# Optimization experiments

Hardware: AMD Instinct MI355X
Metric: run time of the kernel (lower is better)

## Reference

```python
import jax, jax.numpy as jnp
import numpy as np

N_RAYS = 131072
N_SAMPLES = 128
FEAT_DIM = 3
FAR_DELTA = 1e10  # sentinel delta appended for the last sample, as in the torch code


def setup_inputs() -> dict:
    key = jax.random.key(0)
    k1, k2, k3 = jax.random.split(key, 3)
    # densities are non-negative (output of e.g. relu/softplus in NeRF)
    density = jax.random.uniform(k1, (N_RAYS, N_SAMPLES), dtype=jnp.float32) * 2.0
    feature = jax.random.uniform(k2, (N_RAYS, N_SAMPLES, FEAT_DIM), dtype=jnp.float32)
    # monotonically increasing per-ray sample depths: near + cumsum(uniform bins)
    bins = jax.random.uniform(k3, (N_RAYS, N_SAMPLES), dtype=jnp.float32) * 0.05 + 0.01
    depth_values = 1.0 + jnp.cumsum(bins, axis=1)
    return {"density": density, "feature": feature, "depth_values": depth_values}


def reference(density, feature, depth_values):
    # deltas: consecutive depth differences, with a huge last delta (torch.cat(..., 1e10*ones))
    deltas = jnp.concatenate(
        [depth_values[:, 1:] - depth_values[:, :-1],
         jnp.full_like(depth_values[:, :1], FAR_DELTA)],
        axis=-1,
    )  # [N, S]
    att = jnp.exp(-density * deltas)              # exp(-sigma_i * delta_i), [N, S]
    # inclusive prefix product, matching the loop: T[i] = T[i-1]*exp(-sigma_i*delta_i)
    T = jnp.cumprod(att, axis=1)                  # [N, S]
    weights = T * (1.0 - att)                     # [N, S]
    feat_out = jnp.einsum("ns,nsc->nc", weights, feature)      # [N, 3]
    depth_out = jnp.sum(weights * depth_values, axis=1)         # [N]
    return feat_out, depth_out
```

## Files before the change

### kernel.cpp

```cpp
#include <hip/hip_runtime.h>

#define N_RAYS    131072
#define N_SAMPLES 128
#define FAR_DELTA 1e10f

__global__ __launch_bounds__(256) void VolumeRenderer_57612691308835_kernel(
    const float* __restrict__ density,
    const float* __restrict__ feature,
    const float* __restrict__ depth,
    float* __restrict__ out_feat,
    float* __restrict__ out_depth)
{
    const int wave = threadIdx.x >> 6;
    const int lane = threadIdx.x & 63;
    const int ray  = (blockIdx.x << 2) + wave;
    if (ray >= N_RAYS) return;

    const int  s0   = lane << 1;
    const long base = (long)ray * N_SAMPLES;

    const float2 den = *(const float2*)(density + base + s0);
    const float2 dep = *(const float2*)(depth   + base + s0);
    const float* fp  = feature + (base + s0) * 3;
    const float2 f01 = *(const float2*)(fp);
    const float2 f23 = *(const float2*)(fp + 2);
    const float2 f45 = *(const float2*)(fp + 4);

    const float d_next = __shfl_down(dep.x, 1);
    const float delta0 = dep.y - dep.x;
    const float delta1 = (lane == 63) ? FAR_DELTA : (d_next - dep.y);

    const float att0 = __expf(-den.x * delta0);
    const float att1 = __expf(-den.y * delta1);

    float scan = att0 * att1;
    #pragma unroll
    for (int off = 1; off < 64; off <<= 1) {
        const float v = __shfl_up(scan, off);
        scan *= (lane >= off) ? v : 1.0f;
    }
    float excl = __shfl_up(scan, 1);
    if (lane == 0) excl = 1.0f;

    const float T0 = excl * att0;
    const float T1 = T0   * att1;
    const float w0 = T0 * (1.0f - att0);
    const float w1 = T1 * (1.0f - att1);

    float fx = w0 * f01.x + w1 * f23.y;
    float fy = w0 * f01.y + w1 * f45.x;
    float fz = w0 * f23.x + w1 * f45.y;
    float dd = w0 * dep.x + w1 * dep.y;

    #pragma unroll
    for (int off = 32; off >= 1; off >>= 1) {
        fx += __shfl_xor(fx, off);
        fy += __shfl_xor(fy, off);
        fz += __shfl_xor(fz, off);
        dd += __shfl_xor(dd, off);
    }

    if (lane == 0) {
        out_feat[ray * 3 + 0] = fx;
        out_feat[ray * 3 + 1] = fy;
        out_feat[ray * 3 + 2] = fz;
        out_depth[ray]        = dd;
    }
}

extern "C" void kernel_launch(void* const* d_in, const int* in_sizes, int n_in,
                              void* d_out, int out_size, void* d_ws, size_t ws_size,
                              hipStream_t stream) {
    const float* density = (const float*)d_in[0];
    const float* feature = (const float*)d_in[1];
    const float* depth   = (const float*)d_in[2];

    float* out_feat  = (float*)d_out;
    float* out_depth = (float*)d_out + (long)N_RAYS * 3;

    const int rays_per_block = 4;
    const int grid = N_RAYS / rays_per_block;
    VolumeRenderer_57612691308835_kernel<<<grid, 256, 0, stream>>>(
        density, feature, depth, out_feat, out_depth);
}
```

Before: 349.9 us.

## Rewrite renderer as persistent waves with LDS transpose, DPP scans and double-buffered loads

Each wave now handles 32 rays over 8 iterations, issuing coalesced float4 global loads that are double-buffered in registers and transposed through LDS so each lane owns 8 contiguous samples. The per-ray scan and reduction run across 16-lane rows using DPP row shifts instead of 64-lane shuffles, and the four outputs are spread across lanes so they are stored in parallel. This aims to cut load instruction count, shuffle latency and per-block launch overhead. In exchange it uses a lot of LDS per block and adds bank-padding complexity.

```diff
diff --git a/kernel.cpp b/kernel.cpp
--- a/kernel.cpp
+++ b/kernel.cpp
@@ -4,68 +4,174 @@
 #define N_SAMPLES 128
 #define FAR_DELTA 1e10f
 
-__global__ __launch_bounds__(256) void VolumeRenderer_57612691308835_kernel(
+#define NBLOCKS   1024
+
+#define ROW_SHL(n) (0x100 + (n))
+#define ROW_SHR(n) (0x110 + (n))
+#define QPERM(a,b,c,d) ((a) | ((b) << 2) | ((c) << 4) | ((d) << 6))
+
+template <int CTRL>
+__device__ __forceinline__ float dpp_f(float v, float ident) {
+    return __int_as_float(__builtin_amdgcn_update_dpp(
+        __float_as_int(ident), __float_as_int(v), CTRL, 0xF, 0xF, false));
+}
+
+#define WAVE_LDS  13312
+#define FEAT_STR  112
+#define DD_STR    48
+#define DEN_OFF   7168
+#define DEP_OFF   10240
+
+__device__ __forceinline__ int feat_woff(int lane, int c) {
+    const int q  = c * 64 + lane;
+    const int gg = q / 96;
+    const int r  = q - gg * 96;
+    const int pp = r / 6;
+    const int cc = r - pp * 6;
+    return gg * (16 * FEAT_STR) + pp * FEAT_STR + cc * 16;
+}
+__device__ __forceinline__ int dd_woff(int lane, int c, int regionOff) {
+    const int q  = c * 64 + lane;
+    const int gg = q >> 5;
+    const int r  = q & 31;
+    const int pp = r >> 1;
+    const int cc = r & 1;
+    return regionOff + gg * (16 * DD_STR) + pp * DD_STR + cc * 16;
+}
+
+
+#define LOADM(F0,F1,F2,F3,F4,F5,DN0,DN1,DP0,DP1,IT) do {                     \
+    const int fo_ = (IT) * 384, dd_ = (IT) * 128;                            \
+    F0 = fG[fo_];       F1 = fG[fo_ + 64];   F2 = fG[fo_ + 128];             \
+    F3 = fG[fo_ + 192]; F4 = fG[fo_ + 256];  F5 = fG[fo_ + 320];             \
+    DN0 = dnG[dd_];     DN1 = dnG[dd_ + 64];                                 \
+    DP0 = dpG[dd_];     DP1 = dpG[dd_ + 64];                                 \
+} while (0)
+
+#define PROCM(F0,F1,F2,F3,F4,F5,DN0,DN1,DP0,DP1,IT) do {                     \
+    \
+    *(float4*)(wlds + wf0) = F0;  *(float4*)(wlds + wf1) = F1;               \
+    *(float4*)(wlds + wf2) = F2;  *(float4*)(wlds + wf3) = F3;               \
+    *(float4*)(wlds + wf4) = F4;  *(float4*)(wlds + wf5) = F5;               \
+    *(float4*)(wlds + wdn0) = DN0; *(float4*)(wlds + wdn1) = DN1;            \
+    *(float4*)(wlds + wdp0) = DP0; *(float4*)(wlds + wdp1) = DP1;            \
+                  \
+    const float4 dn0 = *(const float4*)(dnR);                                \
+    const float4 dn1 = *(const float4*)(dnR + 16);                           \
+    const float4 dp0 = *(const float4*)(dpR);                                \
+    const float4 dp1 = *(const float4*)(dpR + 16);                           \
+    const float4 f0 = *(const float4*)(fR);                                  \
+    const float4 f1 = *(const float4*)(fR + 16);                             \
+    const float4 f2 = *(const float4*)(fR + 32);                             \
+    const float4 f3 = *(const float4*)(fR + 48);                             \
+    const float4 f4 = *(const float4*)(fR + 64);                             \
+    const float4 f5 = *(const float4*)(fR + 80);                             \
+        \
+    const float dnext = dpp_f<ROW_SHL(1)>(dp0.x, 0.0f);                      \
+    const float d7 = (p == 15) ? FAR_DELTA : (dnext - dp1.w);                \
+    const float a0 = __expf(-dn0.x * (dp0.y - dp0.x));                       \
+    const float a1 = __expf(-dn0.y * (dp0.z - dp0.y));                       \
+    const float a2 = __expf(-dn0.z * (dp0.w - dp0.z));                       \
+    const float a3 = __expf(-dn0.w * (dp1.x - dp0.w));                       \
+    const float a4 = __expf(-dn1.x * (dp1.y - dp1.x));                       \
+    const float a5 = __expf(-dn1.y * (dp1.z - dp1.y));                       \
+    const float a6 = __expf(-dn1.z * (dp1.w - dp1.z));                       \
+    const float a7 = __expf(-dn1.w * d7);                                    \
+    \
+    float s = ((a0 * a1) * (a2 * a3)) * ((a4 * a5) * (a6 * a7));             \
+    s *= dpp_f<ROW_SHR(1)>(s, 1.0f);                                         \
+    s *= dpp_f<ROW_SHR(2)>(s, 1.0f);                                         \
+    s *= dpp_f<ROW_SHR(4)>(s, 1.0f);                                         \
+    s *= dpp_f<ROW_SHR(8)>(s, 1.0f);                                         \
+    float T = dpp_f<ROW_SHR(1)>(s, 1.0f);        \
+    T *= a0; const float w0 = T * (1.0f - a0);                               \
+    T *= a1; const float w1 = T * (1.0f - a1);                               \
+    T *= a2; const float w2 = T * (1.0f - a2);                               \
+    T *= a3; const float w3 = T * (1.0f - a3);                               \
+    T *= a4; const float w4 = T * (1.0f - a4);                               \
+    T *= a5; const float w5 = T * (1.0f - a5);                               \
+    T *= a6; const float w6 = T * (1.0f - a6);                               \
+    T *= a7; const float w7 = T * (1.0f - a7);                               \
+    float fx = w0*f0.x + w1*f0.w + w2*f1.z + w3*f2.y                         \
+             + w4*f3.x + w5*f3.w + w6*f4.z + w7*f5.y;                        \
+    float fy = w0*f0.y + w1*f1.x + w2*f1.w + w3*f2.z                         \
+             + w4*f3.y + w5*f4.x + w6*f4.w + w7*f5.z;                        \
+    float fz = w0*f0.z + w1*f1.y + w2*f2.x + w3*f2.w                         \
+             + w4*f3.z + w5*f4.y + w6*f5.x + w7*f5.w;                        \
+    float dd = w0*dp0.x + w1*dp0.y + w2*dp0.z + w3*dp0.w                     \
+             + w4*dp1.x + w5*dp1.y + w6*dp1.z + w7*dp1.w;                    \
+                \
+    fx += dpp_f<ROW_SHL(8)>(fx, 0.0f);                                       \
+    fy += dpp_f<ROW_SHL(8)>(fy, 0.0f);                                       \
+    fz += dpp_f<ROW_SHL(8)>(fz, 0.0f);                                       \
+    dd += dpp_f<ROW_SHL(8)>(dd, 0.0f);                                       \
+    fx += dpp_f<ROW_SHL(4)>(fx, 0.0f);                                       \
+    fy += dpp_f<ROW_SHL(4)>(fy, 0.0f);                                       \
+    fz += dpp_f<ROW_SHL(4)>(fz, 0.0f);                                       \
+    dd += dpp_f<ROW_SHL(4)>(dd, 0.0f);                                       \
+    const bool o1 = (p & 1);                                                 \
+    const float sA = o1 ? fx : fy;                                           \
+    const float rA = dpp_f<QPERM(1, 0, 3, 2)>(sA, 0.0f);                     \
+    float fy2 = fy, fx2 = fx;                                                \
+    if (o1) fy2 += rA; else fx2 += rA;                                       \
+    const float sB = o1 ? fz : dd;                                           \
+    const float rB = dpp_f<QPERM(1, 0, 3, 2)>(sB, 0.0f);                     \
+    float dd2 = dd, fz2 = fz;                                                \
+    if (o1) dd2 += rB; else fz2 += rB;                                       \
+    const float own = (p & 2) ? (o1 ? dd2 : fz2) : (o1 ? fy2 : fx2);         \
+    const float sC  = (p & 2) ? (o1 ? fy2 : fx2) : (o1 ? dd2 : fz2);         \
+    const float rC  = dpp_f<QPERM(2, 3, 0, 1)>(sC, 0.0f);                    \
+    const float res = own + rC;                                              \
+    const int ray = (int)wray + (IT) * 4 + g;                                \
+    if (p < 3)       out_feat[ray * 3 + p] = res;                            \
+    else if (p == 3) out_depth[ray] = res;                                   \
+} while (0)
+
+#define LOAD_A(IT) LOADM(fA0,fA1,fA2,fA3,fA4,fA5,dnA0,dnA1,dpA0,dpA1,IT)
+#define LOAD_B(IT) LOADM(fB0,fB1,fB2,fB3,fB4,fB5,dnB0,dnB1,dpB0,dpB1,IT)
+#define PROC_A(IT) PROCM(fA0,fA1,fA2,fA3,fA4,fA5,dnA0,dnA1,dpA0,dpA1,IT)
+#define PROC_B(IT) PROCM(fB0,fB1,fB2,fB3,fB4,fB5,dnB0,dnB1,dpB0,dpB1,IT)
+
+__global__ __launch_bounds__(256, 3) void VolumeRenderer_57612691308835_kernel(
     const float* __restrict__ density,
     const float* __restrict__ feature,
     const float* __restrict__ depth,
     float* __restrict__ out_feat,
     float* __restrict__ out_depth)
 {
-    const int wave = threadIdx.x >> 6;
-    const int lane = threadIdx.x & 63;
-    const int ray  = (blockIdx.x << 2) + wave;
-    if (ray >= N_RAYS) return;
+    __shared__ char lds[4 * WAVE_LDS];
 
-    const int  s0   = lane << 1;
-    const long base = (long)ray * N_SAMPLES;
+    const int tid  = threadIdx.x;
+    const int wave = tid >> 6;
+    const int lane = tid & 63;
+    const int p    = lane & 15;
+    const int g    = lane >> 4;
 
-    const float2 den = *(const float2*)(density + base + s0);
-    const float2 dep = *(const float2*)(depth   + base + s0);
-    const float* fp  = feature + (base + s0) * 3;
-    const float2 f01 = *(const float2*)(fp);
-    const float2 f23 = *(const float2*)(fp + 2);
-    const float2 f45 = *(const float2*)(fp + 4);
+    char* wlds = lds + wave * WAVE_LDS;
 
-    const float d_next = __shfl_down(dep.x, 1);
-    const float delta0 = dep.y - dep.x;
-    const float delta1 = (lane == 63) ? FAR_DELTA : (d_next - dep.y);
+    char* fR  = wlds + lane * FEAT_STR;
+    char* dnR = wlds + DEN_OFF + lane * DD_STR;
+    char* dpR = wlds + DEP_OFF + lane * DD_STR;
 
-    const float att0 = __expf(-den.x * delta0);
-    const float att1 = __expf(-den.y * delta1);
+    const int wf0 = feat_woff(lane, 0), wf1 = feat_woff(lane, 1);
+    const int wf2 = feat_woff(lane, 2), wf3 = feat_woff(lane, 3);
+    const int wf4 = feat_woff(lane, 4), wf5 = feat_woff(lane, 5);
+    const int wdn0 = dd_woff(lane, 0, DEN_OFF), wdn1 = dd_woff(lane, 1, DEN_OFF);
+    const int wdp0 = dd_woff(lane, 0, DEP_OFF), wdp1 = dd_woff(lane, 1, DEP_OFF);
 
-    float scan = att0 * att1;
-    #pragma unroll
-    for (int off = 1; off < 64; off <<= 1) {
-        const float v = __shfl_up(scan, off);
-        scan *= (lane >= off) ? v : 1.0f;
-    }
-    float excl = __shfl_up(scan, 1);
-    if (lane == 0) excl = 1.0f;
+    const long wray = ((long)blockIdx.x * 4 + wave) * 32;
+    const float4* fG  = (const float4*)feature + wray * 96 + lane;
+    const float4* dnG = (const float4*)density + wray * 32 + lane;
+    const float4* dpG = (const float4*)depth   + wray * 32 + lane;
 
-    const float T0 = excl * att0;
-    const float T1 = T0   * att1;
-    const float w0 = T0 * (1.0f - att0);
-    const float w1 = T1 * (1.0f - att1);
+    float4 fA0, fA1, fA2, fA3, fA4, fA5, dnA0, dnA1, dpA0, dpA1;
+    float4 fB0, fB1, fB2, fB3, fB4, fB5, dnB0, dnB1, dpB0, dpB1;
 
-    float fx = w0 * f01.x + w1 * f23.y;
-    float fy = w0 * f01.y + w1 * f45.x;
-    float fz = w0 * f23.x + w1 * f45.y;
-    float dd = w0 * dep.x + w1 * dep.y;
-
-    #pragma unroll
-    for (int off = 32; off >= 1; off >>= 1) {
-        fx += __shfl_xor(fx, off);
-        fy += __shfl_xor(fy, off);
-        fz += __shfl_xor(fz, off);
-        dd += __shfl_xor(dd, off);
-    }
-
-    if (lane == 0) {
-        out_feat[ray * 3 + 0] = fx;
-        out_feat[ray * 3 + 1] = fy;
-        out_feat[ray * 3 + 2] = fz;
-        out_depth[ray]        = dd;
-    }
+    LOAD_A(0);
+    LOAD_B(1);  PROC_A(0);  LOAD_A(2);  PROC_B(1);
+    LOAD_B(3);  PROC_A(2);  LOAD_A(4);  PROC_B(3);
+    LOAD_B(5);  PROC_A(4);  LOAD_A(6);  PROC_B(5);
+    LOAD_B(7);  PROC_A(6);              PROC_B(7);
 }
 
 extern "C" void kernel_launch(void* const* d_in, const int* in_sizes, int n_in,
@@ -78,8 +184,6 @@
     float* out_feat  = (float*)d_out;
     float* out_depth = (float*)d_out + (long)N_RAYS * 3;
 
-    const int rays_per_block = 4;
-    const int grid = N_RAYS / rays_per_block;
-    VolumeRenderer_57612691308835_kernel<<<grid, 256, 0, stream>>>(
+    VolumeRenderer_57612691308835_kernel<<<NBLOCKS, 256, 0, stream>>>(
         density, feature, depth, out_feat, out_depth);
 }
```

After: 354.4 us. About the same (+1.3%).
